# Kernel tuning notes

Hardware: AMD Instinct MI355X
Metric: run time of the kernel (lower is better)

The kernel has to match this reference:

```python
import jax, jax.numpy as jnp
import numpy as np

WS = 8          # window_size
NH = 8          # num_heads
IQKV = 128      # inner_qk_v_dim
IQKC = 32       # inner_qk_c_dim
IVV = 64        # inner_v_v_dim
EPS = 1e-6
B, HH, WW, DV, DC = 2, 224, 224, 256, 64


def _rmsnorm(x, g):
    return x * jax.lax.rsqrt(jnp.mean(x * x, axis=-1, keepdims=True) + EPS) * g


def _window(x):
    # (b, h, w, d) -> (b, Wh, Ww, ws*ws, d)
    b, h, w, d = x.shape
    x = x.reshape(b, h // WS, WS, w // WS, WS, d).transpose(0, 1, 3, 2, 4, 5)
    return x.reshape(b, h // WS, w // WS, WS * WS, d)


def _unwindow(x, h, w):
    # (b, N, ws*ws, d) -> (b, h, w, d)
    b, _, _, d = x.shape
    x = x.reshape(b, h // WS, w // WS, WS, WS, d).transpose(0, 1, 3, 2, 4, 5)
    return x.reshape(b, h, w, d)


def _source_qkv(V, C, Wqk_v, bqk_v, g_v, Wqk_c, bqk_c, g_c, Wv):
    Vw, Cw = _window(V), _window(C)          # (b, Wh, Ww, n, d)
    b, Wh, Ww, n, _ = Vw.shape
    N = Wh * Ww
    Vavg, Cavg = Vw.mean(-2), Cw.mean(-2)
    qk_v = _rmsnorm(Vavg @ Wqk_v + bqk_v, g_v)   # (b, Wh, Ww, 2*IQKV)
    qk_c = _rmsnorm(Cavg @ Wqk_c + bqk_c, g_c)   # (b, Wh, Ww, 2*IQKC)
    # 'b Wh Ww (H e) -> b H (Wh Ww) e' then chunk2 along e
    qk_v = qk_v.reshape(b, N, NH, -1).transpose(0, 2, 1, 3)
    qk_c = qk_c.reshape(b, N, NH, -1).transpose(0, 2, 1, 3)
    ev, ec = qk_v.shape[-1] // 2, qk_c.shape[-1] // 2
    qv, kv = qk_v[..., :ev], qk_v[..., ev:]
    qc, kc = qk_c[..., :ec], qk_c[..., ec:]
    # value projection: 'b Wh Ww n (e H) -> b H (Wh Ww) (n e)'
    e = IVV // NH
    Vv = (Vw @ Wv).reshape(b, N, n, e, NH).transpose(0, 4, 1, 2, 3).reshape(b, NH, N, n * e)
    return qv, kv, qc, kc, Vv, (Wh, Ww)


def _forward(values0, coords0, values1, coords1,
             Wqk_v, bqk_v, g_v, Wqk_c, bqk_c, g_c, Wv, Wback):
    parts = [_source_qkv(V, C, Wqk_v, bqk_v, g_v, Wqk_c, bqk_c, g_c, Wv)
             for V, C in ((values0, coords0), (values1, coords1))]
    qv = jnp.concatenate([p[0] for p in parts], axis=2)
    kv = jnp.concatenate([p[1] for p in parts], axis=2)
    qc = jnp.concatenate([p[2] for p in parts], axis=2)
    kc = jnp.concatenate([p[3] for p in parts], axis=2)
    Vv = jnp.concatenate([p[4] for p in parts], axis=2)
    scores = (jnp.einsum('bhqe,bhke->bhqk', qv, kv) / jnp.sqrt(jnp.float32(IQKV))
              + jnp.einsum('bhqe,bhke->bhqk', qc, kc) / jnp.sqrt(jnp.float32(IQKC)))
    A = jax.nn.softmax(scores, axis=-1)            # (b, H, N, N)
    rw = jnp.einsum('bhqk,bhkf->bhqf', A, Vv)      # (b, H, N, n*e)
    b, _, N, _ = rw.shape
    n, e = WS * WS, IVV // NH
    # 'b H N (n e) -> b N n (e H)'
    rw = rw.reshape(b, NH, N, n, e).transpose(0, 2, 3, 4, 1).reshape(b, N, n, e * NH)
    rw = rw @ Wback                                # (b, N, n, Dv)
    outs, off = [], 0
    for (V, _), p in zip(((values0, coords0), (values1, coords1)), parts):
        Wh, Ww = p[5]
        Ns = Wh * Ww
        outs.append(_unwindow(rw[:, off:off + Ns], Wh * WS, Ww * WS))
        off += Ns
    return tuple(outs)


def setup_inputs() -> dict:
    key = jax.random.key(0)
    ks = jax.random.split(key, 8)
    s = 0.02
    return {
        'values0': jax.random.normal(ks[0], (B, HH, WW, DV), jnp.float32),
        'coords0': jax.random.normal(ks[1], (B, HH, WW, DC), jnp.float32),
        'values1': jax.random.normal(ks[2], (B, HH, WW, DV), jnp.float32),
        'coords1': jax.random.normal(ks[3], (B, HH, WW, DC), jnp.float32),
        'Wqk_v': s * jax.random.normal(ks[4], (DV, 2 * IQKV), jnp.float32),
        'bqk_v': jnp.zeros((2 * IQKV,), jnp.float32),
        'g_v': jnp.ones((2 * IQKV,), jnp.float32),
        'Wqk_c': s * jax.random.normal(ks[5], (DC, 2 * IQKC), jnp.float32),
        'bqk_c': jnp.zeros((2 * IQKC,), jnp.float32),
        'g_c': jnp.ones((2 * IQKC,), jnp.float32),
        'Wv': s * jax.random.normal(ks[6], (DV, IVV), jnp.float32),
        'Wback': s * jax.random.normal(ks[7], (IVV, DV), jnp.float32),
    }


def reference(values0, coords0, values1, coords1,
              Wqk_v, bqk_v, g_v, Wqk_c, bqk_c, g_c, Wv, Wback):
    return _forward(values0, coords0, values1, coords1,
                    Wqk_v, bqk_v, g_v, Wqk_c, bqk_c, g_c, Wv, Wback)
```

## Files before the change

### kernel.cpp

```cpp
#include <hip/hip_runtime.h>

#define NSRC 784
#define NTOT 1568
#define NHD 8
#define DVC 256
#define DCC 64
#define D20 20
#define FDIM 512
#define OUT_PER_SRC 25690112

typedef short s16x8 __attribute__((ext_vector_type(8)));
typedef unsigned short u16x8 __attribute__((ext_vector_type(8)));
typedef unsigned short u16x4 __attribute__((ext_vector_type(4)));
typedef float f32x4 __attribute__((ext_vector_type(4)));
typedef float f32x16 __attribute__((ext_vector_type(16)));
typedef unsigned u32x4 __attribute__((ext_vector_type(4)));

#define LOG2E 1.4426950408889634f

__device__ __forceinline__ unsigned short f2bf(float x) {
    unsigned u = __float_as_uint(x);
    unsigned r = (u + 0x7FFFu + ((u >> 16) & 1u)) >> 16;
    return (unsigned short)r;
}

__device__ __forceinline__ unsigned cvt_pk_bf16(float lo, float hi) {
    unsigned r;
    asm volatile("v_cvt_pk_bf16_f32 %0, %1, %2" : "=v"(r) : "v"(lo), "v"(hi));
    return r;
}

__device__ __forceinline__ void split_bf(float x, unsigned short& hi, unsigned short& lo) {
    unsigned short h = f2bf(x);
    float hf = __uint_as_float(((unsigned)h) << 16);
    hi = h;
    lo = f2bf(x - hf);
}

__device__ __forceinline__ void permlane32_swap(unsigned& a, unsigned& b) {
    asm volatile("v_permlane32_swap_b32 %0, %1" : "+v"(a), "+v"(b));
}

__global__ __launch_bounds__(256) void kz_zero(unsigned short* __restrict__ p) {
    size_t i = (size_t)blockIdx.x * 256 + threadIdx.x;
    u16x8 z = (u16x8)0;
    *(u16x8*)&p[i * 8] = z;
}

__global__ __launch_bounds__(256) void k0c_wvpack(
    const float* __restrict__ Wv, unsigned short* __restrict__ Wvp) {
    int idx = blockIdx.x * 256 + threadIdx.x;
    int j = idx & 7, lane = (idx >> 3) & 63, hl = (idx >> 9) & 1;
    int c = (idx >> 10) & 7, mi = idx >> 13;
    int e = mi * 16 + (lane & 15);
    int dd = c * 32 + (lane >> 4) * 8 + j;
    unsigned short h, l;
    split_bf(Wv[dd * DCC + e], h, l);
    Wvp[idx] = hl ? l : h;
}

__global__ __launch_bounds__(256) void k0b_wback(
    const float* __restrict__ Wb, unsigned short* __restrict__ Wp) {
    int idx = blockIdx.x * 256 + threadIdx.x;
    int jj = idx & 7, lane = (idx >> 3) & 63, hl = (idx >> 9) & 1;
    int kc = (idx >> 10) & 1, mt = idx >> 11;
    int c = mt * 16 + (lane & 15);
    int j = kc * 32 + (lane >> 4) * 8 + jj;
    unsigned short h, l;
    split_bf(Wb[j * 256 + c], h, l);
    Wp[idx] = hl ? l : h;
}

__global__ __launch_bounds__(256) void k1c_avg(
    const float* __restrict__ c0, const float* __restrict__ c1,
    float* __restrict__ Cavg) {
    int wi = blockIdx.x * 4 + (threadIdx.x >> 6);
    int d = threadIdx.x & 63;
    int b = wi / NTOT, N = wi % NTOT;
    int src = N / NSRC, nloc = N % NSRC;
    int wh = nloc / 28, ww = nloc % 28;
    const float* __restrict__ C = src ? c1 : c0;
    int pbase = (b * 224 + wh * 8) * 224 + ww * 8;
    float s = 0.f;
#pragma unroll 8
    for (int p = 0; p < 64; ++p)
        s += C[(size_t)(pbase + (p >> 3) * 224 + (p & 7)) * DCC + d];
    Cavg[(size_t)wi * DCC + d] = s * 0.015625f;
}

__global__ __launch_bounds__(256) void k2_qk(
    const float* __restrict__ Vavg, const float* __restrict__ Cavg,
    const float* __restrict__ Wqkv, const float* __restrict__ bqkv, const float* __restrict__ gv,
    const float* __restrict__ Wqkc, const float* __restrict__ bqkc, const float* __restrict__ gc,
    unsigned short* __restrict__ Qp, unsigned short* __restrict__ Kp) {
    __shared__ float xv[DVC];
    __shared__ float xc[DCC];
    __shared__ float wred[4];
    int blk = blockIdx.x;
    int b = blk / NTOT, N = blk % NTOT;
    int t = threadIdx.x;
    int tile = N >> 5, l31 = N & 31;
    xv[t] = Vavg[(size_t)blk * DVC + t];
    if (t < DCC) xc[t] = Cavg[(size_t)blk * DCC + t];
    __syncthreads();
    float yv = bqkv[t];
#pragma unroll 4
    for (int d = 0; d < DVC; ++d) yv += xv[d] * Wqkv[d * 256 + t];
    float ss = yv * yv;
#pragma unroll
    for (int off = 32; off; off >>= 1) ss += __shfl_xor(ss, off, 64);
    if ((t & 63) == 0) wred[t >> 6] = ss;
    __syncthreads();
    float tot = wred[0] + wred[1] + wred[2] + wred[3];
    float rv = rsqrtf(tot * (1.f / 256.f) + 1e-6f);
    float yn = yv * rv * gv[t];
    int h = t >> 5, c = t & 31;
    int bh = b * NHD + h;
    {
        int isq = (c < 16);
        int d = isq ? c : c - 16;
        float val = isq ? yn * (0.088388347648318447f * LOG2E) : yn;
        unsigned short h16, l16;
        split_bf(val, h16, l16);
        int hh = d >> 3, j = d & 7;
        size_t base = ((size_t)(bh * 49 + tile) * 4) * 512 + (size_t)(hh * 32 + l31) * 8 + j;
        unsigned short* dst = isq ? Qp : Kp;
        dst[base] = h16;
        dst[base + 1024] = l16;
    }
    if (t < DCC) {
        float yc = bqkc[t];
#pragma unroll 4
        for (int d = 0; d < DCC; ++d) yc += xc[d] * Wqkc[d * 64 + t];
        float sc = yc * yc;
#pragma unroll
        for (int off = 32; off; off >>= 1) sc += __shfl_xor(sc, off, 64);
        float rc = rsqrtf(sc * (1.f / 64.f) + 1e-6f);
        float ycn = yc * rc * gc[t];
        int h2 = t >> 3, c2 = t & 7;
        int bh2 = b * NHD + h2;
        int isq = (c2 < 4);
        int dd = isq ? c2 : c2 - 4;
        float val = isq ? ycn * (0.17677669529663687f * LOG2E) : ycn;
        unsigned short h16, l16;
        split_bf(val, h16, l16);
        size_t base = ((size_t)(bh2 * 49 + tile) * 4 + 1) * 512 + (size_t)l31 * 8 + dd;
        unsigned short* dst = isq ? Qp : Kp;
        dst[base] = h16;
        dst[base + 1024] = l16;
    }
}

__global__ __launch_bounds__(256) void k3_vv(
    const float* __restrict__ v0, const float* __restrict__ v1,
    const unsigned short* __restrict__ Wvp,
    unsigned short* __restrict__ Vvb, float* __restrict__ Vavg) {
    __shared__ unsigned short eb[64 * 66];
    __shared__ float avgw[1024];
    int blk = blockIdx.x;
    int b = blk / NTOT, N = blk % NTOT;
    int src = N / NSRC, nloc = N % NSRC;
    int wh = nloc / 28, ww = nloc % 28;
    const float* __restrict__ V = src ? v1 : v0;
    int t = threadIdx.x;
    int w = t >> 6, lane = t & 63;
    int lm = lane & 15, lk = lane >> 4;
    int px = w * 16 + lm;
    int pbase = (b * 224 + wh * 8) * 224 + ww * 8;
    const float* __restrict__ xrow =
        V + (size_t)(pbase + (px >> 3) * 224 + (px & 7)) * DVC + lk * 8;

    f32x4 acc[4];
#pragma unroll
    for (int mi = 0; mi < 4; ++mi) acc[mi] = (f32x4)0.f;

#pragma unroll
    for (int c = 0; c < 8; ++c) {
        float4 x0 = *(const float4*)&xrow[c * 32];
        float4 x1 = *(const float4*)&xrow[c * 32 + 4];
        float xv8[8] = {x0.x, x0.y, x0.z, x0.w, x1.x, x1.y, x1.z, x1.w};
        u16x8 bhu, blu;
#pragma unroll
        for (int j = 0; j < 8; ++j) {
            unsigned short hq, lq;
            split_bf(xv8[j], hq, lq);
            bhu[j] = hq; blu[j] = lq;
        }
        s16x8 xhi = __builtin_bit_cast(s16x8, bhu);
        s16x8 xlo = __builtin_bit_cast(s16x8, blu);
        float sv[8] = {xv8[0], xv8[1], xv8[2], xv8[3], xv8[4], xv8[5], xv8[6], xv8[7]};
#pragma unroll
        for (int off = 1; off <= 8; off <<= 1)
#pragma unroll
            for (int j = 0; j < 8; ++j) sv[j] += __shfl_xor(sv[j], off, 64);
        if (lm == 0) {
#pragma unroll
            for (int j = 0; j < 8; ++j)
                avgw[w * 256 + c * 32 + lk * 8 + j] = sv[j];
        }
#pragma unroll
        for (int mi = 0; mi < 4; ++mi) {
            const unsigned short* Wf = Wvp + (size_t)((mi * 8 + c) * 2) * 512 + lane * 8;
            s16x8 Ah = *(const s16x8*)&Wf[0];
            s16x8 Al = *(const s16x8*)&Wf[512];
            acc[mi] = __builtin_amdgcn_mfma_f32_16x16x32_bf16(Ah, xlo, acc[mi], 0, 0, 0);
            acc[mi] = __builtin_amdgcn_mfma_f32_16x16x32_bf16(Al, xhi, acc[mi], 0, 0, 0);
            acc[mi] = __builtin_amdgcn_mfma_f32_16x16x32_bf16(Ah, xhi, acc[mi], 0, 0, 0);
        }
    }
#pragma unroll
    for (int mi = 0; mi < 4; ++mi) {
#pragma unroll
        for (int r = 0; r < 4; ++r) {
            int e = mi * 16 + lk * 4 + r;
            eb[px * 66 + e] = f2bf(acc[mi][r]);
        }
    }
    __syncthreads();
    unsigned short* dst = Vvb + (size_t)blk * 4096;
#pragma unroll
    for (int i = 0; i < 2; ++i) {
        int flat16 = i * 256 + t;
        int f3 = flat16 >> 6;
        int h = (flat16 >> 3) & 7;
        int px8 = (flat16 & 7) * 8;
        u16x8 vv;
#pragma unroll
        for (int u = 0; u < 8; ++u) vv[u] = eb[(px8 + u) * 66 + f3 * 8 + h];
        *(u16x8*)&dst[flat16 * 8] = vv;
    }
    Vavg[(size_t)blk * DVC + t] =
        (avgw[t] + avgw[256 + t] + avgw[512 + t] + avgw[768 + t]) * 0.015625f;
}

__global__ __launch_bounds__(256) void k3b_pack(
    const unsigned short* __restrict__ Vvb, unsigned short* __restrict__ Vp) {
    __shared__ unsigned short tile[32 * 576];
    int kt = blockIdx.x, bh = blockIdx.y;
    int b = bh >> 3, h = bh & 7;
    int t = threadIdx.x;
#pragma unroll
    for (int it = 0; it < 8; ++it) {
        int flat = it * 256 + t;
        int r5 = flat >> 6;
        int c = flat & 63;
        int f3 = c >> 3, px8 = (c & 7) * 8;
        const unsigned short* s =
            Vvb + ((size_t)(b * NTOT + kt * 32 + r5) * 8 + f3) * 512 + h * 64 + px8;
        *(u16x8*)&tile[r5 * 576 + f3 * 72 + px8] = *(const u16x8*)s;
    }
    __syncthreads();
    unsigned short* dst = Vp + ((size_t)bh * 49 + kt) * 16384;
#pragma unroll
    for (int it = 0; it < 8; ++it) {
        int flato = it * 256 + t;
        int lane = flato & 63;
        int kh = (flato >> 6) & 1;
        int sub = (flato >> 7) & 3;
        int w = flato >> 9;
        int l31 = lane & 31, hh = lane >> 5;
        int f = w * 128 + sub * 32 + l31;
        int kbase = kh * 16 + hh * 8;
        u16x8 v;
#pragma unroll
        for (int j = 0; j < 8; ++j)
            v[j] = tile[(kbase + j) * 576 + (f & 7) * 72 + (f >> 3)];
        *(u16x8*)&dst[(size_t)flato * 8] = v;
    }
}

__global__ __launch_bounds__(256) void k4_attn(
    const unsigned short* __restrict__ Qp, const unsigned short* __restrict__ Kp,
    const unsigned short* __restrict__ Vp, float* __restrict__ rw) {
    __shared__ float ebuf[32 * 132];
    int wg = blockIdx.x;
    int qt = wg >> 4, bh = wg & 15;
    int q0 = qt * 32;
    int t = threadIdx.x;
    int w = t >> 6, lane = t & 63;
    int l31 = lane & 31, hh = lane >> 5;

    const unsigned short* __restrict__ Qpb = Qp + ((size_t)(bh * 49 + qt) * 4) * 512 + lane * 8;
    const unsigned short* __restrict__ Kpb = Kp + (size_t)bh * 49 * 2048 + lane * 8;
    const unsigned short* __restrict__ Vpb = Vp + (size_t)bh * 49 * 16384 + lane * 8;

    s16x8 qa0 = *(const s16x8*)&Qpb[0];
    s16x8 qa1 = *(const s16x8*)&Qpb[512];
    s16x8 ql0 = *(const s16x8*)&Qpb[1024];
    s16x8 ql1 = *(const s16x8*)&Qpb[1536];

    s16x8 ka0 = *(const s16x8*)&Kpb[0];
    s16x8 ka1 = *(const s16x8*)&Kpb[512];
    s16x8 kl0 = *(const s16x8*)&Kpb[1024];
    s16x8 kl1 = *(const s16x8*)&Kpb[1536];

    float m = -1e30f, lsum = 0.f;
    f32x16 acc[4];
#pragma unroll
    for (int s = 0; s < 4; ++s) acc[s] = (f32x16)0.f;

    for (int kt = 0; kt < NTOT / 32; ++kt) {
        const unsigned short* Vtile = Vpb + (size_t)kt * 16384 + (w * 8) * 512;
        s16x8 va[8];
#pragma unroll
        for (int fr = 0; fr < 8; ++fr)
            va[fr] = *(const s16x8*)&Vtile[fr * 512];
        int ktn = (kt < 48) ? kt + 1 : 48;
        const unsigned short* Ktn = Kpb + (size_t)ktn * 2048;
        s16x8 kn0 = *(const s16x8*)&Ktn[0];
        s16x8 kn1 = *(const s16x8*)&Ktn[512];
        s16x8 kn2 = *(const s16x8*)&Ktn[1024];
        s16x8 kn3 = *(const s16x8*)&Ktn[1536];

        f32x16 sacc = (f32x16)0.f;
        sacc = __builtin_amdgcn_mfma_f32_32x32x16_bf16(kl0, qa0, sacc, 0, 0, 0);
        sacc = __builtin_amdgcn_mfma_f32_32x32x16_bf16(ka0, ql0, sacc, 0, 0, 0);
        sacc = __builtin_amdgcn_mfma_f32_32x32x16_bf16(ka0, qa0, sacc, 0, 0, 0);
        sacc = __builtin_amdgcn_mfma_f32_32x32x16_bf16(kl1, qa1, sacc, 0, 0, 0);
        sacc = __builtin_amdgcn_mfma_f32_32x32x16_bf16(ka1, ql1, sacc, 0, 0, 0);
        sacc = __builtin_amdgcn_mfma_f32_32x32x16_bf16(ka1, qa1, sacc, 0, 0, 0);

        float t0 = fmaxf(fmaxf(sacc[0], sacc[1]), sacc[2]);
        float t1 = fmaxf(fmaxf(sacc[3], sacc[4]), sacc[5]);
        float t2 = fmaxf(fmaxf(sacc[6], sacc[7]), sacc[8]);
        float t3 = fmaxf(fmaxf(sacc[9], sacc[10]), sacc[11]);
        float t4 = fmaxf(fmaxf(sacc[12], sacc[13]), sacc[14]);
        float u0 = fmaxf(fmaxf(t0, t1), t2);
        float u1 = fmaxf(t3, t4);
        float tmax = fmaxf(fmaxf(u0, u1), sacc[15]);
        tmax = fmaxf(tmax, __shfl_xor(tmax, 32, 64));
        if (__any(tmax > m + 11.5f)) {
            float mn = fmaxf(m, tmax);
            float sc = exp2f(m - mn);
#pragma unroll
            for (int s = 0; s < 4; ++s) acc[s] = acc[s] * sc;
            lsum *= sc;
            m = mn;
        }
        unsigned P2[8];
        float tsum = 0.f;
#pragma unroll
        for (int j = 0; j < 8; ++j) {
            float pa = exp2f(sacc[2 * j] - m);
            float pb = exp2f(sacc[2 * j + 1] - m);
            tsum += pa + pb;
            P2[j] = cvt_pk_bf16(pa, pb);
        }
        lsum += tsum + __shfl_xor(tsum, 32, 64);
        permlane32_swap(P2[0], P2[2]);
        permlane32_swap(P2[1], P2[3]);
        permlane32_swap(P2[4], P2[6]);
        permlane32_swap(P2[5], P2[7]);
        u32x4 b0u, b1u;
        b0u[0] = P2[0]; b0u[1] = P2[1]; b0u[2] = P2[2]; b0u[3] = P2[3];
        b1u[0] = P2[4]; b1u[1] = P2[5]; b1u[2] = P2[6]; b1u[3] = P2[7];
        s16x8 pb0 = __builtin_bit_cast(s16x8, b0u);
        s16x8 pb1 = __builtin_bit_cast(s16x8, b1u);

#pragma unroll
        for (int sub = 0; sub < 4; ++sub) {
            acc[sub] = __builtin_amdgcn_mfma_f32_32x32x16_bf16(va[2 * sub],     pb0, acc[sub], 0, 0, 0);
            acc[sub] = __builtin_amdgcn_mfma_f32_32x32x16_bf16(va[2 * sub + 1], pb1, acc[sub], 0, 0, 0);
        }
        ka0 = kn0; ka1 = kn1; kl0 = kn2; kl1 = kn3;
    }

    float inv = 1.f / lsum;
    float* rwg = rw + ((size_t)bh * NTOT + q0) * FDIM;
#pragma unroll
    for (int c = 0; c < 4; ++c) {
        __syncthreads();
        if (w == c) {
#pragma unroll
            for (int sub = 0; sub < 4; ++sub) {
#pragma unroll
                for (int r = 0; r < 16; ++r) {
                    int fl = sub * 32 + (r & 3) + 8 * (r >> 2) + 4 * hh;
                    ebuf[l31 * 132 + fl] = acc[sub][r] * inv;
                }
            }
        }
        __syncthreads();
        int qr = t >> 3, cb = (t & 7) * 16;
#pragma unroll
        for (int j = 0; j < 4; ++j) {
            *(float4*)&rwg[(size_t)qr * FDIM + c * 128 + cb + j * 4] =
                *(const float4*)&ebuf[qr * 132 + cb + j * 4];
        }
    }
}

__global__ __launch_bounds__(256) void k5_back(
    const float* __restrict__ rw, const unsigned short* __restrict__ Wp,
    float* __restrict__ out) {
    __shared__ unsigned short SB[2 * 64 * 72];
    unsigned short* BhL = SB;
    unsigned short* BlL = SB + 64 * 72;
    int blk = blockIdx.x;
    int b = blk / NTOT, N = blk % NTOT;
    int src = N / NSRC, nloc = N % NSRC;
    int wh = nloc / 28, ww = nloc % 28;
    int t = threadIdx.x;
    int w = t >> 6, lane = t & 63;
    int lm = lane & 15, lk = lane >> 4;
    int pbase = (b * 224 + wh * 8) * 224 + ww * 8;

#pragma unroll
    for (int i = 0; i < 4; ++i) {
        int flat4 = i * 256 + t;
        int h = flat4 >> 7;
        int f0 = (flat4 & 127) * 4;
        float4 v = *(const float4*)&rw[((size_t)(b * NHD + h) * NTOT + N) * FDIM + f0];
        int n = f0 >> 3;
        int ebase = f0 & 7;
        float vv[4] = {v.x, v.y, v.z, v.w};
#pragma unroll
        for (int u = 0; u < 4; ++u) {
            int j8 = ebase + u;
            unsigned short h16, l16;
            split_bf(vv[u], h16, l16);
            int col = ((j8 ^ (n & 7)) << 3) | h;
            BhL[n * 72 + col] = h16;
            BlL[n * 72 + col] = l16;
        }
    }
    __syncthreads();

    f32x4 acc[4][4];
#pragma unroll
    for (int mi = 0; mi < 4; ++mi)
#pragma unroll
        for (int nt = 0; nt < 4; ++nt) acc[mi][nt] = (f32x4)0.f;

    const unsigned short* Wpw = Wp + (size_t)(w * 4) * 2048 + lane * 8;
#pragma unroll
    for (int kc = 0; kc < 2; ++kc) {
        s16x8 Ah[4], Al[4], Bh4[4], Bl4[4];
#pragma unroll
        for (int mi = 0; mi < 4; ++mi) {
            int base = mi * 2048 + kc * 1024;
            Ah[mi] = *(const s16x8*)&Wpw[base];
            Al[mi] = *(const s16x8*)&Wpw[base + 512];
        }
#pragma unroll
        for (int nt = 0; nt < 4; ++nt) {
            int n = nt * 16 + lm;
            int addr = n * 72 + (((kc * 4 + lk) ^ (n & 7)) << 3);
            Bh4[nt] = *(const s16x8*)&BhL[addr];
            Bl4[nt] = *(const s16x8*)&BlL[addr];
        }
#pragma unroll
        for (int mi = 0; mi < 4; ++mi)
#pragma unroll
            for (int nt = 0; nt < 4; ++nt) {
                acc[mi][nt] = __builtin_amdgcn_mfma_f32_16x16x32_bf16(Ah[mi], Bl4[nt], acc[mi][nt], 0, 0, 0);
                acc[mi][nt] = __builtin_amdgcn_mfma_f32_16x16x32_bf16(Al[mi], Bh4[nt], acc[mi][nt], 0, 0, 0);
                acc[mi][nt] = __builtin_amdgcn_mfma_f32_16x16x32_bf16(Ah[mi], Bh4[nt], acc[mi][nt], 0, 0, 0);
            }
    }

    float* eb = (float*)SB;
    float* outp = out + (size_t)src * OUT_PER_SRC;
#pragma unroll
    for (int ch = 0; ch < 4; ++ch) {
        __syncthreads();
        if (w == ch) {
#pragma unroll
            for (int mi = 0; mi < 4; ++mi)
#pragma unroll
                for (int nt = 0; nt < 4; ++nt)
#pragma unroll
                    for (int r = 0; r < 4; ++r) {
                        int n = nt * 16 + lm;
                        int cl = mi * 16 + lk * 4 + r;
                        eb[n * 68 + cl] = acc[mi][nt][r];
                    }
        }
        __syncthreads();
#pragma unroll
        for (int i = 0; i < 4; ++i) {
            int fl4 = i * 256 + t;
            int n = fl4 >> 4, c4 = (fl4 & 15) * 4;
            int opix = pbase + (n >> 3) * 224 + (n & 7);
            *(float4*)&outp[(size_t)opix * DVC + ch * 64 + c4] =
                *(const float4*)&eb[n * 68 + c4];
        }
    }
}

extern "C" void kernel_launch(void* const* d_in, const int* in_sizes, int n_in,
                              void* d_out, int out_size, void* d_ws, size_t ws_size,
                              hipStream_t stream) {
    const float* v0   = (const float*)d_in[0];
    const float* c0   = (const float*)d_in[1];
    const float* v1   = (const float*)d_in[2];
    const float* c1   = (const float*)d_in[3];
    const float* Wqkv = (const float*)d_in[4];
    const float* bqkv = (const float*)d_in[5];
    const float* gv   = (const float*)d_in[6];
    const float* Wqkc = (const float*)d_in[7];
    const float* bqkc = (const float*)d_in[8];
    const float* gc   = (const float*)d_in[9];
    const float* Wv   = (const float*)d_in[10];
    const float* Wbk  = (const float*)d_in[11];

    float* ws = (float*)d_ws;
    float* rw   = ws;
    float* Vavg = ws;
    float* Cavg = ws + 802816;
    unsigned short* Qp   = (unsigned short*)(ws + 12845056);
    unsigned short* Kp   = (unsigned short*)(ws + 13647872);
    unsigned short* Wvp  = (unsigned short*)(ws + 14450688);
    unsigned short* Vvb  = (unsigned short*)(ws + 14467072);
    unsigned short* Vp   = (unsigned short*)(ws + 20889600);
    unsigned short* Wp   = (unsigned short*)(ws + 27312128);

    float* outp = (float*)d_out;

    kz_zero   <<<1568, 256, 0, stream>>>(Qp);
    k0c_wvpack<<<256, 256, 0, stream>>>(Wv, Wvp);
    k0b_wback <<<256, 256, 0, stream>>>(Wbk, Wp);
    k3_vv     <<<2 * NTOT, 256, 0, stream>>>(v0, v1, Wvp, Vvb, Vavg);
    k1c_avg   <<<784, 256, 0, stream>>>(c0, c1, Cavg);
    k2_qk     <<<2 * NTOT, 256, 0, stream>>>(Vavg, Cavg, Wqkv, bqkv, gv, Wqkc, bqkc, gc, Qp, Kp);
    k3b_pack  <<<dim3(49, 16), 256, 0, stream>>>(Vvb, Vp);
    k4_attn   <<<784, 256, 0, stream>>>(Qp, Kp, Vp, rw);
    k5_back   <<<2 * NTOT, 256, 0, stream>>>(rw, Wp, outp);
}
```

Baseline: 347.5 us.

## Split QK score computation across waves and share softmax probabilities via LDS

Previously every wave recomputed the full 32x32 QK^T score tile and its softmax for each key tile, which duplicated work four times. Now each of the four waves computes scores for a different key tile in a group of four. The waves exchange row max and sum through shared memory and share the bf16 probability fragments through LDS, then each wave runs the PV MFMAs for all four tiles. The leftover 49th tile is handled in an epilogue, and exp2f is replaced by raw v_exp_f32. This costs two block barriers per group of four tiles and extra LDS traffic.

```diff
diff --git a/kernel.cpp b/kernel.cpp
--- a/kernel.cpp
+++ b/kernel.cpp
@@ -27,6 +27,12 @@
 __device__ __forceinline__ unsigned cvt_pk_bf16(float lo, float hi) {
     unsigned r;
     asm volatile("v_cvt_pk_bf16_f32 %0, %1, %2" : "=v"(r) : "v"(lo), "v"(hi));
+    return r;
+}
+
+__device__ __forceinline__ float fexp2(float x) {
+    float r;
+    asm("v_exp_f32 %0, %1" : "=v"(r) : "v"(x));
     return r;
 }
 
@@ -272,7 +278,13 @@
 __global__ __launch_bounds__(256) void k4_attn(
     const unsigned short* __restrict__ Qp, const unsigned short* __restrict__ Kp,
     const unsigned short* __restrict__ Vp, float* __restrict__ rw) {
-    __shared__ float ebuf[32 * 132];
+    __shared__ char smem[16896];
+    u32x4* PB0 = (u32x4*)smem;
+    u32x4* PB1 = (u32x4*)(smem + 4096);
+    float* maxbuf = (float*)(smem + 8192);
+    float* sumbuf = (float*)(smem + 8704);
+    float* ebuf = (float*)smem;
+
     int wg = blockIdx.x;
     int qt = wg >> 4, bh = wg & 15;
     int q0 = qt * 32;
@@ -289,29 +301,21 @@
     s16x8 ql0 = *(const s16x8*)&Qpb[1024];
     s16x8 ql1 = *(const s16x8*)&Qpb[1536];
 
-    s16x8 ka0 = *(const s16x8*)&Kpb[0];
-    s16x8 ka1 = *(const s16x8*)&Kpb[512];
-    s16x8 kl0 = *(const s16x8*)&Kpb[1024];
-    s16x8 kl1 = *(const s16x8*)&Kpb[1536];
+    {
+    }
+    const unsigned short* Kt0 = Kpb + (size_t)w * 2048;
+    s16x8 ka0 = *(const s16x8*)&Kt0[0];
+    s16x8 ka1 = *(const s16x8*)&Kt0[512];
+    s16x8 kl0 = *(const s16x8*)&Kt0[1024];
+    s16x8 kl1 = *(const s16x8*)&Kt0[1536];
 
     float m = -1e30f, lsum = 0.f;
     f32x16 acc[4];
 #pragma unroll
     for (int s = 0; s < 4; ++s) acc[s] = (f32x16)0.f;
 
-    for (int kt = 0; kt < NTOT / 32; ++kt) {
-        const unsigned short* Vtile = Vpb + (size_t)kt * 16384 + (w * 8) * 512;
-        s16x8 va[8];
-#pragma unroll
-        for (int fr = 0; fr < 8; ++fr)
-            va[fr] = *(const s16x8*)&Vtile[fr * 512];
-        int ktn = (kt < 48) ? kt + 1 : 48;
-        const unsigned short* Ktn = Kpb + (size_t)ktn * 2048;
-        s16x8 kn0 = *(const s16x8*)&Ktn[0];
-        s16x8 kn1 = *(const s16x8*)&Ktn[512];
-        s16x8 kn2 = *(const s16x8*)&Ktn[1024];
-        s16x8 kn3 = *(const s16x8*)&Ktn[1536];
-
+    for (int st = 0; st < 12; ++st) {
+        int kt0 = st * 4;
         f32x16 sacc = (f32x16)0.f;
         sacc = __builtin_amdgcn_mfma_f32_32x32x16_bf16(kl0, qa0, sacc, 0, 0, 0);
         sacc = __builtin_amdgcn_mfma_f32_32x32x16_bf16(ka0, ql0, sacc, 0, 0, 0);
@@ -319,33 +323,142 @@
         sacc = __builtin_amdgcn_mfma_f32_32x32x16_bf16(kl1, qa1, sacc, 0, 0, 0);
         sacc = __builtin_amdgcn_mfma_f32_32x32x16_bf16(ka1, ql1, sacc, 0, 0, 0);
         sacc = __builtin_amdgcn_mfma_f32_32x32x16_bf16(ka1, qa1, sacc, 0, 0, 0);
+        int ktn = (st < 11) ? (st + 1) * 4 + w : 48;
+        const unsigned short* Ktn = Kpb + (size_t)ktn * 2048;
+        s16x8 kn0 = *(const s16x8*)&Ktn[0];
+        s16x8 kn1 = *(const s16x8*)&Ktn[512];
+        s16x8 kn2 = *(const s16x8*)&Ktn[1024];
+        s16x8 kn3 = *(const s16x8*)&Ktn[1536];
+        const unsigned short* Vst = Vpb + (size_t)kt0 * 16384 + (w * 8) * 512;
+        s16x8 vaA[8], vaB[8];
+#pragma unroll
+        for (int fr = 0; fr < 8; ++fr) vaA[fr] = *(const s16x8*)&Vst[fr * 512];
+#pragma unroll
+        for (int fr = 0; fr < 8; ++fr) vaB[fr] = *(const s16x8*)&Vst[16384 + fr * 512];
 
         float t0 = fmaxf(fmaxf(sacc[0], sacc[1]), sacc[2]);
         float t1 = fmaxf(fmaxf(sacc[3], sacc[4]), sacc[5]);
         float t2 = fmaxf(fmaxf(sacc[6], sacc[7]), sacc[8]);
         float t3 = fmaxf(fmaxf(sacc[9], sacc[10]), sacc[11]);
         float t4 = fmaxf(fmaxf(sacc[12], sacc[13]), sacc[14]);
-        float u0 = fmaxf(fmaxf(t0, t1), t2);
-        float u1 = fmaxf(t3, t4);
-        float tmax = fmaxf(fmaxf(u0, u1), sacc[15]);
+        float tmax = fmaxf(fmaxf(fmaxf(t0, t1), fmaxf(t2, t3)), fmaxf(t4, sacc[15]));
+        tmax = fmaxf(tmax, __shfl_xor(tmax, 32, 64));
+        if (hh == 0) maxbuf[w * 32 + l31] = tmax;
+        __syncthreads();
+        float bm = fmaxf(fmaxf(maxbuf[l31], maxbuf[32 + l31]),
+                         fmaxf(maxbuf[64 + l31], maxbuf[96 + l31]));
+        if (__any(bm > m + 11.5f)) {
+            float mn = fmaxf(m, bm);
+            float sc = fexp2(m - mn);
+#pragma unroll
+            for (int s = 0; s < 4; ++s) acc[s] = acc[s] * sc;
+            lsum *= sc;
+            m = mn;
+        }
+        unsigned P2[8];
+        float ts0 = 0.f, ts1 = 0.f;
+#pragma unroll
+        for (int j = 0; j < 8; ++j) {
+            float pa = fexp2(sacc[2 * j] - m);
+            float pb = fexp2(sacc[2 * j + 1] - m);
+            ts0 += pa; ts1 += pb;
+            P2[j] = cvt_pk_bf16(pa, pb);
+        }
+        float tsum = ts0 + ts1;
+        tsum += __shfl_xor(tsum, 32, 64);
+        if (hh == 0) sumbuf[w * 32 + l31] = tsum;
+        permlane32_swap(P2[0], P2[2]);
+        permlane32_swap(P2[1], P2[3]);
+        permlane32_swap(P2[4], P2[6]);
+        permlane32_swap(P2[5], P2[7]);
+        u32x4 b0u, b1u;
+        b0u[0] = P2[0]; b0u[1] = P2[1]; b0u[2] = P2[2]; b0u[3] = P2[3];
+        b1u[0] = P2[4]; b1u[1] = P2[5]; b1u[2] = P2[6]; b1u[3] = P2[7];
+        PB0[w * 64 + lane] = b0u;
+        PB1[w * 64 + lane] = b1u;
+        __syncthreads();
+        lsum += sumbuf[l31] + sumbuf[32 + l31] + sumbuf[64 + l31] + sumbuf[96 + l31];
+
+        {
+            s16x8 pb0 = __builtin_bit_cast(s16x8, PB0[0 * 64 + lane]);
+            s16x8 pb1 = __builtin_bit_cast(s16x8, PB1[0 * 64 + lane]);
+#pragma unroll
+            for (int sub = 0; sub < 4; ++sub) {
+                acc[sub] = __builtin_amdgcn_mfma_f32_32x32x16_bf16(vaA[2 * sub],     pb0, acc[sub], 0, 0, 0);
+                acc[sub] = __builtin_amdgcn_mfma_f32_32x32x16_bf16(vaA[2 * sub + 1], pb1, acc[sub], 0, 0, 0);
+            }
+        }
+#pragma unroll
+        for (int fr = 0; fr < 8; ++fr) vaA[fr] = *(const s16x8*)&Vst[2 * 16384 + fr * 512];
+        {
+            s16x8 pb0 = __builtin_bit_cast(s16x8, PB0[1 * 64 + lane]);
+            s16x8 pb1 = __builtin_bit_cast(s16x8, PB1[1 * 64 + lane]);
+#pragma unroll
+            for (int sub = 0; sub < 4; ++sub) {
+                acc[sub] = __builtin_amdgcn_mfma_f32_32x32x16_bf16(vaB[2 * sub],     pb0, acc[sub], 0, 0, 0);
+                acc[sub] = __builtin_amdgcn_mfma_f32_32x32x16_bf16(vaB[2 * sub + 1], pb1, acc[sub], 0, 0, 0);
+            }
+        }
+#pragma unroll
+        for (int fr = 0; fr < 8; ++fr) vaB[fr] = *(const s16x8*)&Vst[3 * 16384 + fr * 512];
+        {
+            s16x8 pb0 = __builtin_bit_cast(s16x8, PB0[2 * 64 + lane]);
+            s16x8 pb1 = __builtin_bit_cast(s16x8, PB1[2 * 64 + lane]);
+#pragma unroll
+            for (int sub = 0; sub < 4; ++sub) {
+                acc[sub] = __builtin_amdgcn_mfma_f32_32x32x16_bf16(vaA[2 * sub],     pb0, acc[sub], 0, 0, 0);
+                acc[sub] = __builtin_amdgcn_mfma_f32_32x32x16_bf16(vaA[2 * sub + 1], pb1, acc[sub], 0, 0, 0);
+            }
+        }
+        {
+            s16x8 pb0 = __builtin_bit_cast(s16x8, PB0[3 * 64 + lane]);
+            s16x8 pb1 = __builtin_bit_cast(s16x8, PB1[3 * 64 + lane]);
+#pragma unroll
+            for (int sub = 0; sub < 4; ++sub) {
+                acc[sub] = __builtin_amdgcn_mfma_f32_32x32x16_bf16(vaB[2 * sub],     pb0, acc[sub], 0, 0, 0);
+                acc[sub] = __builtin_amdgcn_mfma_f32_32x32x16_bf16(vaB[2 * sub + 1], pb1, acc[sub], 0, 0, 0);
+            }
+        }
+        ka0 = kn0; ka1 = kn1; kl0 = kn2; kl1 = kn3;
+    }
+
+    {
+        f32x16 sacc = (f32x16)0.f;
+        sacc = __builtin_amdgcn_mfma_f32_32x32x16_bf16(kl0, qa0, sacc, 0, 0, 0);
+        sacc = __builtin_amdgcn_mfma_f32_32x32x16_bf16(ka0, ql0, sacc, 0, 0, 0);
+        sacc = __builtin_amdgcn_mfma_f32_32x32x16_bf16(ka0, qa0, sacc, 0, 0, 0);
+        sacc = __builtin_amdgcn_mfma_f32_32x32x16_bf16(kl1, qa1, sacc, 0, 0, 0);
+        sacc = __builtin_amdgcn_mfma_f32_32x32x16_bf16(ka1, ql1, sacc, 0, 0, 0);
+        sacc = __builtin_amdgcn_mfma_f32_32x32x16_bf16(ka1, qa1, sacc, 0, 0, 0);
+        const unsigned short* Vst = Vpb + (size_t)48 * 16384 + (w * 8) * 512;
+        s16x8 vaA[8];
+#pragma unroll
+        for (int fr = 0; fr < 8; ++fr) vaA[fr] = *(const s16x8*)&Vst[fr * 512];
+        float t0 = fmaxf(fmaxf(sacc[0], sacc[1]), sacc[2]);
+        float t1 = fmaxf(fmaxf(sacc[3], sacc[4]), sacc[5]);
+        float t2 = fmaxf(fmaxf(sacc[6], sacc[7]), sacc[8]);
+        float t3 = fmaxf(fmaxf(sacc[9], sacc[10]), sacc[11]);
+        float t4 = fmaxf(fmaxf(sacc[12], sacc[13]), sacc[14]);
+        float tmax = fmaxf(fmaxf(fmaxf(t0, t1), fmaxf(t2, t3)), fmaxf(t4, sacc[15]));
         tmax = fmaxf(tmax, __shfl_xor(tmax, 32, 64));
         if (__any(tmax > m + 11.5f)) {
             float mn = fmaxf(m, tmax);
-            float sc = exp2f(m - mn);
+            float sc = fexp2(m - mn);
 #pragma unroll
             for (int s = 0; s < 4; ++s) acc[s] = acc[s] * sc;
             lsum *= sc;
             m = mn;
         }
         unsigned P2[8];
-        float tsum = 0.f;
+        float ts0 = 0.f, ts1 = 0.f;
 #pragma unroll
         for (int j = 0; j < 8; ++j) {
-            float pa = exp2f(sacc[2 * j] - m);
-            float pb = exp2f(sacc[2 * j + 1] - m);
-            tsum += pa + pb;
+            float pa = fexp2(sacc[2 * j] - m);
+            float pb = fexp2(sacc[2 * j + 1] - m);
+            ts0 += pa; ts1 += pb;
             P2[j] = cvt_pk_bf16(pa, pb);
         }
+        float tsum = ts0 + ts1;
         lsum += tsum + __shfl_xor(tsum, 32, 64);
         permlane32_swap(P2[0], P2[2]);
         permlane32_swap(P2[1], P2[3]);
@@ -356,13 +469,11 @@
         b1u[0] = P2[4]; b1u[1] = P2[5]; b1u[2] = P2[6]; b1u[3] = P2[7];
         s16x8 pb0 = __builtin_bit_cast(s16x8, b0u);
         s16x8 pb1 = __builtin_bit_cast(s16x8, b1u);
-
 #pragma unroll
         for (int sub = 0; sub < 4; ++sub) {
-            acc[sub] = __builtin_amdgcn_mfma_f32_32x32x16_bf16(va[2 * sub],     pb0, acc[sub], 0, 0, 0);
-            acc[sub] = __builtin_amdgcn_mfma_f32_32x32x16_bf16(va[2 * sub + 1], pb1, acc[sub], 0, 0, 0);
-        }
-        ka0 = kn0; ka1 = kn1; kl0 = kn2; kl1 = kn3;
+            acc[sub] = __builtin_amdgcn_mfma_f32_32x32x16_bf16(vaA[2 * sub],     pb0, acc[sub], 0, 0, 0);
+            acc[sub] = __builtin_amdgcn_mfma_f32_32x32x16_bf16(vaA[2 * sub + 1], pb1, acc[sub], 0, 0, 0);
+        }
     }
 
     float inv = 1.f / lsum;
```

Result: slower. 424.3 us (+22.1%).
